# Kernel optimization log

Measured on AMD Instinct MI355X. Metric: run time of the kernel, lower is better.

The kernel has to match this reference:

```python
import jax, jax.numpy as jnp
import numpy as np

H = 64
B = 128
R_PER_G = 1024
P_PER_G = 2048
R = B * R_PER_G      # 131072 routers
P = B * P_PER_G      # 262144 packets
E_PASS = 1048576     # packet -> router
E_TRANS = 1048576    # router -> packet
E_CONN = 524288      # router -> router
NUM_LABELS = 11      # label_max - label_min


def setup_inputs() -> dict:
    key = jax.random.key(0)
    ks = jax.random.split(key, 40)
    f32 = jnp.float32

    def w(k, shape):
        fan_in = shape[0]
        return (jax.random.normal(k, shape, f32) / np.sqrt(fan_in)).astype(f32)

    inp = {}
    # graph node features
    inp['freq'] = jax.random.uniform(ks[0], (P, 1), f32)
    inp['flit'] = jax.random.normal(ks[1], (P, 32), f32)
    inp['op_type'] = jax.random.uniform(ks[2], (R, 4), f32)
    # edge lists (src, dst) per etype
    inp['pass_src'] = jax.random.randint(ks[3], (E_PASS,), 0, P, jnp.int32)
    inp['pass_dst'] = jax.random.randint(ks[4], (E_PASS,), 0, R, jnp.int32)
    inp['transfer_src'] = jax.random.randint(ks[5], (E_TRANS,), 0, R, jnp.int32)
    inp['transfer_dst'] = jax.random.randint(ks[6], (E_TRANS,), 0, P, jnp.int32)
    inp['connect_src'] = jax.random.randint(ks[7], (E_CONN,), 0, R, jnp.int32)
    inp['connect_dst'] = jax.random.randint(ks[8], (E_CONN,), 0, R, jnp.int32)
    # graph id of each router node (batched graphs, contiguous)
    inp['router_gid'] = jnp.repeat(jnp.arange(B, dtype=jnp.int32), R_PER_G)
    # FeatureGen params
    inp['Wf'] = w(ks[10], (1, H));      inp['bf'] = jnp.zeros((H,), f32)
    inp['Wl'] = w(ks[11], (32, H));     inp['bl'] = jnp.zeros((H,), f32)
    inp['Wo'] = w(ks[12], (4, H));      inp['bo'] = jnp.zeros((H,), f32)
    inp['Wfh'] = w(ks[13], (2 * H, H)); inp['bfh'] = jnp.zeros((H,), f32)
    inp['Wfn'] = w(ks[14], (H, H));     inp['bfn'] = jnp.zeros((H,), f32)
    # conv1 / conv2 params
    inp['c1_Wr'] = w(ks[15], (2 * H, H)); inp['c1_br'] = jnp.zeros((H,), f32)
    inp['c1_Wp'] = w(ks[16], (H, H));     inp['c1_bp'] = jnp.zeros((H,), f32)
    inp['c2_Wr'] = w(ks[17], (2 * H, H)); inp['c2_br'] = jnp.zeros((H,), f32)
    inp['c2_Wp'] = w(ks[18], (H, H));     inp['c2_bp'] = jnp.zeros((H,), f32)
    # prediction head
    inp['h1W'] = w(ks[19], (2 * H, H));        inp['h1b'] = jnp.zeros((H,), f32)
    inp['h2W'] = w(ks[20], (H, H));            inp['h2b'] = jnp.zeros((H,), f32)
    inp['h3W'] = w(ks[21], (H, NUM_LABELS));   inp['h3b'] = jnp.zeros((NUM_LABELS,), f32)
    return inp


def _conv(r_feat, p_feat, pass_src, pass_dst, transfer_src, transfer_dst,
          connect_src, connect_dst, Wr, br, Wp, bp):
    relu = jax.nn.relu
    # 'pass': copy_u packet feat, sum at router -> h1
    h1 = jax.ops.segment_sum(p_feat[pass_src], pass_dst, num_segments=R)
    # 'connect': copy_u router feat, sum at router -> h2
    h2 = jax.ops.segment_sum(r_feat[connect_src], connect_dst, num_segments=R)
    # 'transfer': copy_u router feat, mean at packet -> h1
    msum = jax.ops.segment_sum(r_feat[transfer_src], transfer_dst, num_segments=P)
    cnt = jax.ops.segment_sum(jnp.ones((transfer_dst.shape[0],), r_feat.dtype),
                              transfer_dst, num_segments=P)
    pmean = msum / jnp.maximum(cnt, 1.0)[:, None]
    r_out = r_feat + relu(jnp.concatenate([h1, h2], axis=-1) @ Wr + br)
    p_out = p_feat + relu(pmean @ Wp + bp)
    return r_out, p_out


def reference(freq, flit, op_type, pass_src, pass_dst, transfer_src, transfer_dst,
              connect_src, connect_dst, router_gid,
              Wf, bf, Wl, bl, Wo, bo, Wfh, bfh, Wfn, bfn,
              c1_Wr, c1_br, c1_Wp, c1_bp, c2_Wr, c2_br, c2_Wp, c2_bp,
              h1W, h1b, h2W, h2b, h3W, h3b):
    relu = jax.nn.relu
    # FeatureGen
    freq_feat = relu(freq @ Wf + bf)                 # [P, H]
    flit_feat = relu(flit @ Wl + bl)                 # [P, H]
    p_feat = relu(jnp.concatenate([freq_feat, flit_feat], axis=1) @ Wfh + bfh)
    r_feat = relu(relu(op_type @ Wo + bo) @ Wfn + bfn)  # [R, H]
    # two hetero conv layers
    r_feat, p_feat = _conv(r_feat, p_feat, pass_src, pass_dst, transfer_src,
                           transfer_dst, connect_src, connect_dst,
                           c1_Wr, c1_br, c1_Wp, c1_bp)
    r_feat, p_feat = _conv(r_feat, p_feat, pass_src, pass_dst, transfer_src,
                           transfer_dst, connect_src, connect_dst,
                           c2_Wr, c2_br, c2_Wp, c2_bp)
    # per-graph readout over router nodes: sum and max
    emb_sum = jax.ops.segment_sum(r_feat, router_gid, num_segments=B)   # [B, H]
    emb_max = jax.ops.segment_max(r_feat, router_gid, num_segments=B)   # [B, H]
    emb = jnp.concatenate([emb_sum, emb_max], axis=-1)                  # [B, 2H]
    # prediction head
    h = relu(emb @ h1W + h1b)
    h = relu(h @ h2W + h2b)
    pred = h @ h3W + h3b                                                # [B, 11]
    return pred
```

## Files before the change

### kernel.cpp

```cpp
#include <hip/hip_runtime.h>
#include <cstddef>

#define RELU(x) ((x) > 0.f ? (x) : 0.f)

constexpr int PN = 262144;
constexpr int RN = 131072;
constexpr int BN = 128;
constexpr int EPASS = 1048576;
constexpr int ETRANS = 1048576;
constexpr int ECONN = 524288;

__device__ __forceinline__ float bflo(unsigned u) { return __uint_as_float(u << 16); }
__device__ __forceinline__ float bfhi(unsigned u) { return __uint_as_float(u & 0xffff0000u); }
__device__ __forceinline__ unsigned bfpk(float x, float y) {
    unsigned ux = __float_as_uint(x), uy = __float_as_uint(y);
    ux += 0x7fffu + ((ux >> 16) & 1u);
    uy += 0x7fffu + ((uy >> 16) & 1u);
    return (ux >> 16) | (uy & 0xffff0000u);
}

struct Acc8 {
    float a0,a1,a2,a3,a4,a5,a6,a7;
    __device__ __forceinline__ void zero(){a0=a1=a2=a3=a4=a5=a6=a7=0.f;}
    __device__ __forceinline__ void add(uint4 v){
        a0+=bflo(v.x); a1+=bfhi(v.x); a2+=bflo(v.y); a3+=bfhi(v.y);
        a4+=bflo(v.z); a5+=bfhi(v.z); a6+=bflo(v.w); a7+=bfhi(v.w);
    }
    __device__ __forceinline__ void scale(float s){a0*=s;a1*=s;a2*=s;a3*=s;a4*=s;a5*=s;a6*=s;a7*=s;}
    __device__ __forceinline__ uint4 pack() const {
        return make_uint4(bfpk(a0,a1), bfpk(a2,a3), bfpk(a4,a5), bfpk(a6,a7));
    }
};

__global__ __launch_bounds__(256) void k_hist3(
    const int* __restrict__ pass_dst, const int* __restrict__ cn_dst,
    const int* __restrict__ tr_dst, int* __restrict__ deg3)
{
    int e = blockIdx.x * 256 + threadIdx.x;
    if (e < EPASS)                  atomicAdd(&deg3[pass_dst[e]], 1);
    else if (e < EPASS + ECONN)     atomicAdd(&deg3[RN + cn_dst[e - EPASS]], 1);
    else                            atomicAdd(&deg3[2*RN + tr_dst[e - EPASS - ECONN]], 1);
}

__global__ __launch_bounds__(1024) void k_scan_a(
    const int* __restrict__ deg3, int* __restrict__ rp_pass,
    int* __restrict__ rp_conn, int* __restrict__ rp_trans, int* __restrict__ bsum)
{
    int gb = blockIdx.x, t = threadIdx.x;
    const int* d; int* rp; int off;
    if (gb < 128)      { d = deg3;        rp = rp_pass;  off = gb * 1024; }
    else if (gb < 256) { d = deg3 + RN;   rp = rp_conn;  off = (gb-128) * 1024; }
    else               { d = deg3 + 2*RN; rp = rp_trans; off = (gb-256) * 1024; }
    int v = d[off + t];
    __shared__ int ss[1024];
    ss[t] = v;
    __syncthreads();
    for (int dd = 1; dd < 1024; dd <<= 1) {
        int u = (t >= dd) ? ss[t-dd] : 0;
        __syncthreads();
        ss[t] += u;
        __syncthreads();
    }
    rp[off + t] = ss[t] - v;
    if (t == 1023) bsum[gb] = ss[t];
}

__global__ __launch_bounds__(256) void k_scan_b(int* __restrict__ bsum)
{
    int s = blockIdx.x, t = threadIdx.x;
    int base = (s == 0) ? 0 : (s == 1 ? 128 : 256);
    int n = (s == 2) ? 256 : 128;
    int v = (t < n) ? bsum[base + t] : 0;
    __shared__ int ss[256];
    ss[t] = v;
    __syncthreads();
    for (int dd = 1; dd < 256; dd <<= 1) {
        int u = (t >= dd) ? ss[t-dd] : 0;
        __syncthreads();
        ss[t] += u;
        __syncthreads();
    }
    if (t < n) bsum[base + t] = ss[t] - v;
}

__global__ __launch_bounds__(1024) void k_scan_c(
    int* __restrict__ rp_pass, int* __restrict__ rp_conn, int* __restrict__ rp_trans,
    const int* __restrict__ bsum)
{
    int gb = blockIdx.x, t = threadIdx.x;
    int* rp; int off;
    if (gb < 128)      { rp = rp_pass;  off = gb * 1024; }
    else if (gb < 256) { rp = rp_conn;  off = (gb-128) * 1024; }
    else               { rp = rp_trans; off = (gb-256) * 1024; }
    rp[off + t] += bsum[gb];
    if (t == 0) {
        if (gb == 0)   rp_pass[RN]  = EPASS;
        if (gb == 128) rp_conn[RN]  = ECONN;
        if (gb == 256) rp_trans[PN] = ETRANS;
    }
}

__global__ __launch_bounds__(256) void k_fill3(
    const int* __restrict__ pass_src, const int* __restrict__ pass_dst,
    const int* __restrict__ cn_src,   const int* __restrict__ cn_dst,
    const int* __restrict__ tr_src,   const int* __restrict__ tr_dst,
    const int* __restrict__ rp_pass, const int* __restrict__ rp_conn,
    const int* __restrict__ rp_trans, int* __restrict__ cur3,
    int* __restrict__ csrc_pass, int* __restrict__ csrc_conn, int* __restrict__ csrc_trans)
{
    int e = blockIdx.x * 256 + threadIdx.x;
    if (e < EPASS) {
        int d = pass_dst[e];
        int pos = atomicAdd(&cur3[d], 1);
        csrc_pass[rp_pass[d] + pos] = pass_src[e];
    } else if (e < EPASS + ECONN) {
        int ee = e - EPASS;
        int d = cn_dst[ee];
        int pos = atomicAdd(&cur3[RN + d], 1);
        csrc_conn[rp_conn[d] + pos] = cn_src[ee];
    } else {
        int ee = e - EPASS - ECONN;
        int d = tr_dst[ee];
        int pos = atomicAdd(&cur3[2*RN + d], 1);
        csrc_trans[rp_trans[d] + pos] = tr_src[ee];
    }
}

__global__ __launch_bounds__(256) void k_gather_r(
    const ushort* __restrict__ pf, const ushort* __restrict__ rfv,
    const int* __restrict__ rp_pass, const int* __restrict__ csrc_pass,
    const int* __restrict__ rp_conn, const int* __restrict__ csrc_conn,
    ushort* __restrict__ h12)
{
    int tid = blockIdx.x * 256 + threadIdx.x;
    int n = tid >> 3, c = tid & 7;
    Acc8 a;
    {
        int beg = rp_pass[n], end = rp_pass[n + 1];
        a.zero();
        int j = beg;
        for (; j + 4 <= end; j += 4) {
            int s0 = csrc_pass[j], s1 = csrc_pass[j+1], s2 = csrc_pass[j+2], s3 = csrc_pass[j+3];
            uint4 v0 = *(const uint4*)(pf + (size_t)s0 * 64 + c * 8);
            uint4 v1 = *(const uint4*)(pf + (size_t)s1 * 64 + c * 8);
            uint4 v2 = *(const uint4*)(pf + (size_t)s2 * 64 + c * 8);
            uint4 v3 = *(const uint4*)(pf + (size_t)s3 * 64 + c * 8);
            a.add(v0); a.add(v1); a.add(v2); a.add(v3);
        }
        for (; j < end; ++j) {
            int s0 = csrc_pass[j];
            a.add(*(const uint4*)(pf + (size_t)s0 * 64 + c * 8));
        }
        *(uint4*)(h12 + (size_t)n * 128 + c * 8) = a.pack();
    }
    {
        int beg = rp_conn[n], end = rp_conn[n + 1];
        a.zero();
        int j = beg;
        for (; j + 4 <= end; j += 4) {
            int s0 = csrc_conn[j], s1 = csrc_conn[j+1], s2 = csrc_conn[j+2], s3 = csrc_conn[j+3];
            uint4 v0 = *(const uint4*)(rfv + (size_t)s0 * 64 + c * 8);
            uint4 v1 = *(const uint4*)(rfv + (size_t)s1 * 64 + c * 8);
            uint4 v2 = *(const uint4*)(rfv + (size_t)s2 * 64 + c * 8);
            uint4 v3 = *(const uint4*)(rfv + (size_t)s3 * 64 + c * 8);
            a.add(v0); a.add(v1); a.add(v2); a.add(v3);
        }
        for (; j < end; ++j) {
            int s0 = csrc_conn[j];
            a.add(*(const uint4*)(rfv + (size_t)s0 * 64 + c * 8));
        }
        *(uint4*)(h12 + (size_t)n * 128 + 64 + c * 8) = a.pack();
    }
}

__global__ __launch_bounds__(256) void k_gather_t(
    const ushort* __restrict__ rfv, const int* __restrict__ rp_trans,
    const int* __restrict__ csrc_trans, ushort* __restrict__ pmean)
{
    int tid = blockIdx.x * 256 + threadIdx.x;
    int n = tid >> 3, c = tid & 7;
    int beg = rp_trans[n], end = rp_trans[n + 1];
    Acc8 a;
    a.zero();
    int j = beg;
    for (; j + 4 <= end; j += 4) {
        int s0 = csrc_trans[j], s1 = csrc_trans[j+1], s2 = csrc_trans[j+2], s3 = csrc_trans[j+3];
        uint4 v0 = *(const uint4*)(rfv + (size_t)s0 * 64 + c * 8);
        uint4 v1 = *(const uint4*)(rfv + (size_t)s1 * 64 + c * 8);
        uint4 v2 = *(const uint4*)(rfv + (size_t)s2 * 64 + c * 8);
        uint4 v3 = *(const uint4*)(rfv + (size_t)s3 * 64 + c * 8);
        a.add(v0); a.add(v1); a.add(v2); a.add(v3);
    }
    for (; j < end; ++j) {
        int s0 = csrc_trans[j];
        a.add(*(const uint4*)(rfv + (size_t)s0 * 64 + c * 8));
    }
    a.scale(1.0f / fmaxf((float)(end - beg), 1.0f));
    *(uint4*)(pmean + (size_t)n * 64 + c * 8) = a.pack();
}

__global__ __launch_bounds__(256) void k_pfeat(
    const float* __restrict__ freq, const float* __restrict__ flit,
    const float* __restrict__ Wf, const float* __restrict__ bf,
    const float* __restrict__ Wl, const float* __restrict__ bl,
    const float* __restrict__ Wfh, const float* __restrict__ bfh,
    ushort* __restrict__ pf)
{
    __shared__ float sWlT[64*32];
    __shared__ float sWfh[128*64];
    __shared__ float sWf[64], sbf[64], sbl[64], sbfh[64];
    for (int i = threadIdx.x; i < 64*32; i += 256) {
        int j = i >> 5, k = i & 31;
        sWlT[i] = Wl[k*64 + j];
    }
    for (int i = threadIdx.x; i < 128*64; i += 256) sWfh[i] = Wfh[i];
    if (threadIdx.x < 64) {
        sWf[threadIdx.x]  = Wf[threadIdx.x];
        sbf[threadIdx.x]  = bf[threadIdx.x];
        sbl[threadIdx.x]  = bl[threadIdx.x];
        sbfh[threadIdx.x] = bfh[threadIdx.x];
    }
    __syncthreads();
    int p = blockIdx.x * 256 + threadIdx.x;
    float fl[32];
    const float4* fsrc = (const float4*)(flit + (size_t)p * 32);
    #pragma unroll
    for (int q = 0; q < 8; ++q) {
        float4 v = fsrc[q];
        fl[q*4+0]=v.x; fl[q*4+1]=v.y; fl[q*4+2]=v.z; fl[q*4+3]=v.w;
    }
    float fr = freq[p];
    float out[64];
    #pragma unroll
    for (int h = 0; h < 64; ++h) out[h] = sbfh[h];
    for (int j = 0; j < 64; ++j) {
        const float* wrow = &sWlT[j*32];
        float a0 = sbl[j], a1 = 0.f, a2 = 0.f, a3 = 0.f;
        #pragma unroll
        for (int k = 0; k < 8; ++k) {
            a0 += fl[k]    * wrow[k];
            a1 += fl[k+8]  * wrow[k+8];
            a2 += fl[k+16] * wrow[k+16];
            a3 += fl[k+24] * wrow[k+24];
        }
        float cj = RELU((a0+a1)+(a2+a3));
        #pragma unroll
        for (int h = 0; h < 64; ++h) out[h] += cj * sWfh[(64+j)*64+h];
    }
    for (int j = 0; j < 64; ++j) {
        float cj = RELU(fr * sWf[j] + sbf[j]);
        #pragma unroll
        for (int h = 0; h < 64; ++h) out[h] += cj * sWfh[j*64+h];
    }
    uint4* op4 = (uint4*)(pf + (size_t)p * 64);
    #pragma unroll
    for (int q = 0; q < 8; ++q) {
        op4[q] = make_uint4(bfpk(RELU(out[8*q+0]), RELU(out[8*q+1])),
                            bfpk(RELU(out[8*q+2]), RELU(out[8*q+3])),
                            bfpk(RELU(out[8*q+4]), RELU(out[8*q+5])),
                            bfpk(RELU(out[8*q+6]), RELU(out[8*q+7])));
    }
}

__global__ __launch_bounds__(256) void k_rfeat(
    const float* __restrict__ op,
    const float* __restrict__ Wo, const float* __restrict__ bo,
    const float* __restrict__ Wfn, const float* __restrict__ bfn,
    ushort* __restrict__ rf)
{
    __shared__ float sWoT[64*4];
    __shared__ float sWfn[64*64], sbo[64], sbfn[64];
    for (int i = threadIdx.x; i < 64*4; i += 256) {
        int j = i >> 2, d = i & 3;
        sWoT[i] = Wo[d*64 + j];
    }
    for (int i = threadIdx.x; i < 64*64; i += 256) sWfn[i] = Wfn[i];
    if (threadIdx.x < 64) { sbo[threadIdx.x] = bo[threadIdx.x]; sbfn[threadIdx.x] = bfn[threadIdx.x]; }
    __syncthreads();
    int r = blockIdx.x * 256 + threadIdx.x;
    float4 o4 = *(const float4*)(op + (size_t)r * 4);
    float out[64];
    #pragma unroll
    for (int h = 0; h < 64; ++h) out[h] = sbfn[h];
    for (int j = 0; j < 64; ++j) {
        const float4 w = *(const float4*)&sWoT[j*4];
        float tj = RELU(o4.x*w.x + o4.y*w.y + o4.z*w.z + o4.w*w.w + sbo[j]);
        #pragma unroll
        for (int h = 0; h < 64; ++h) out[h] += tj * sWfn[j*64+h];
    }
    uint4* op4 = (uint4*)(rf + (size_t)r * 64);
    #pragma unroll
    for (int q = 0; q < 8; ++q) {
        op4[q] = make_uint4(bfpk(RELU(out[8*q+0]), RELU(out[8*q+1])),
                            bfpk(RELU(out[8*q+2]), RELU(out[8*q+3])),
                            bfpk(RELU(out[8*q+4]), RELU(out[8*q+5])),
                            bfpk(RELU(out[8*q+6]), RELU(out[8*q+7])));
    }
}

__global__ __launch_bounds__(256) void k_rupd(
    const ushort* __restrict__ h12,
    const float* __restrict__ Wr, const float* __restrict__ br,
    ushort* __restrict__ rf)
{
    __shared__ float sW[128*64], sb[64];
    for (int i = threadIdx.x; i < 128*64; i += 256) sW[i] = Wr[i];
    if (threadIdx.x < 64) sb[threadIdx.x] = br[threadIdx.x];
    __syncthreads();
    int r = blockIdx.x * 256 + threadIdx.x;
    const uint4* hp = (const uint4*)(h12 + (size_t)r * 128);
    float out[64];
    #pragma unroll
    for (int h = 0; h < 64; ++h) out[h] = sb[h];
    for (int q = 0; q < 16; ++q) {
        uint4 v = hp[q];
        float x0 = bflo(v.x), x1 = bfhi(v.x), x2 = bflo(v.y), x3 = bfhi(v.y);
        float x4 = bflo(v.z), x5 = bfhi(v.z), x6 = bflo(v.w), x7 = bfhi(v.w);
        const float* w = &sW[(8*q)*64];
        #pragma unroll
        for (int h = 0; h < 64; ++h) {
            out[h] += x0*w[h] + x1*w[64+h] + x2*w[128+h] + x3*w[192+h]
                    + x4*w[256+h] + x5*w[320+h] + x6*w[384+h] + x7*w[448+h];
        }
    }
    uint4* rp4 = (uint4*)(rf + (size_t)r * 64);
    #pragma unroll
    for (int q = 0; q < 8; ++q) {
        uint4 cur = rp4[q];
        float c0 = bflo(cur.x) + RELU(out[8*q+0]), c1 = bfhi(cur.x) + RELU(out[8*q+1]);
        float c2 = bflo(cur.y) + RELU(out[8*q+2]), c3 = bfhi(cur.y) + RELU(out[8*q+3]);
        float c4 = bflo(cur.z) + RELU(out[8*q+4]), c5 = bfhi(cur.z) + RELU(out[8*q+5]);
        float c6 = bflo(cur.w) + RELU(out[8*q+6]), c7 = bfhi(cur.w) + RELU(out[8*q+7]);
        rp4[q] = make_uint4(bfpk(c0,c1), bfpk(c2,c3), bfpk(c4,c5), bfpk(c6,c7));
    }
}

__global__ __launch_bounds__(256) void k_pupd(
    const ushort* __restrict__ pmean,
    const float* __restrict__ Wp, const float* __restrict__ bp,
    ushort* __restrict__ pf)
{
    __shared__ float sW[64*64], sb[64];
    for (int i = threadIdx.x; i < 64*64; i += 256) sW[i] = Wp[i];
    if (threadIdx.x < 64) sb[threadIdx.x] = bp[threadIdx.x];
    __syncthreads();
    int p = blockIdx.x * 256 + threadIdx.x;
    const uint4* mp = (const uint4*)(pmean + (size_t)p * 64);
    float out[64];
    #pragma unroll
    for (int h = 0; h < 64; ++h) out[h] = sb[h];
    for (int q = 0; q < 8; ++q) {
        uint4 v = mp[q];
        float x0 = bflo(v.x), x1 = bfhi(v.x), x2 = bflo(v.y), x3 = bfhi(v.y);
        float x4 = bflo(v.z), x5 = bfhi(v.z), x6 = bflo(v.w), x7 = bfhi(v.w);
        const float* w = &sW[(8*q)*64];
        #pragma unroll
        for (int h = 0; h < 64; ++h) {
            out[h] += x0*w[h] + x1*w[64+h] + x2*w[128+h] + x3*w[192+h]
                    + x4*w[256+h] + x5*w[320+h] + x6*w[384+h] + x7*w[448+h];
        }
    }
    uint4* pp4 = (uint4*)(pf + (size_t)p * 64);
    #pragma unroll
    for (int q = 0; q < 8; ++q) {
        uint4 cur = pp4[q];
        float c0 = bflo(cur.x) + RELU(out[8*q+0]), c1 = bfhi(cur.x) + RELU(out[8*q+1]);
        float c2 = bflo(cur.y) + RELU(out[8*q+2]), c3 = bfhi(cur.y) + RELU(out[8*q+3]);
        float c4 = bflo(cur.z) + RELU(out[8*q+4]), c5 = bfhi(cur.z) + RELU(out[8*q+5]);
        float c6 = bflo(cur.w) + RELU(out[8*q+6]), c7 = bfhi(cur.w) + RELU(out[8*q+7]);
        pp4[q] = make_uint4(bfpk(c0,c1), bfpk(c2,c3), bfpk(c4,c5), bfpk(c6,c7));
    }
}

__global__ __launch_bounds__(256) void k_head(
    const ushort* __restrict__ rf,
    const float* __restrict__ h1W, const float* __restrict__ h1b,
    const float* __restrict__ h2W, const float* __restrict__ h2b,
    const float* __restrict__ h3W, const float* __restrict__ h3b,
    float* __restrict__ out)
{
    int b = blockIdx.x;
    int tid = threadIdx.x;
    int h = tid & 63, part = tid >> 6;
    const ushort* base = rf + (size_t)b * 1024 * 64;
    float s = 0.f, m = -3.0e38f;
    #pragma unroll 8
    for (int r = part * 256; r < part * 256 + 256; ++r) {
        float v = bflo((unsigned)base[(size_t)r * 64 + h]);
        s += v;
        m = fmaxf(m, v);
    }
    __shared__ float ssum[4][64], smax[4][64];
    __shared__ float emb[128], hid1[64], hid2[64];
    ssum[part][h] = s;
    smax[part][h] = m;
    __syncthreads();
    if (tid < 64) {
        emb[tid] = ssum[0][tid] + ssum[1][tid] + ssum[2][tid] + ssum[3][tid];
    } else if (tid < 128) {
        int hh = tid - 64;
        emb[64+hh] = fmaxf(fmaxf(smax[0][hh], smax[1][hh]), fmaxf(smax[2][hh], smax[3][hh]));
    }
    __syncthreads();
    if (tid < 64) {
        float a = h1b[tid];
        #pragma unroll
        for (int j = 0; j < 128; ++j) a += emb[j] * h1W[j*64 + tid];
        hid1[tid] = RELU(a);
    }
    __syncthreads();
    if (tid < 64) {
        float a = h2b[tid];
        #pragma unroll
        for (int j = 0; j < 64; ++j) a += hid1[j] * h2W[j*64 + tid];
        hid2[tid] = RELU(a);
    }
    __syncthreads();
    if (tid < 11) {
        float a = h3b[tid];
        #pragma unroll
        for (int j = 0; j < 64; ++j) a += hid2[j] * h3W[j*11 + tid];
        out[(size_t)b * 11 + tid] = a;
    }
}

extern "C" void kernel_launch(void* const* d_in, const int* in_sizes, int n_in,
                              void* d_out, int out_size, void* d_ws, size_t ws_size,
                              hipStream_t stream)
{
    const float* freq = (const float*)d_in[0];
    const float* flit = (const float*)d_in[1];
    const float* op   = (const float*)d_in[2];
    const int* pass_src = (const int*)d_in[3];
    const int* pass_dst = (const int*)d_in[4];
    const int* tr_src   = (const int*)d_in[5];
    const int* tr_dst   = (const int*)d_in[6];
    const int* cn_src   = (const int*)d_in[7];
    const int* cn_dst   = (const int*)d_in[8];
    const float* Wf  = (const float*)d_in[10]; const float* bf  = (const float*)d_in[11];
    const float* Wl  = (const float*)d_in[12]; const float* bl  = (const float*)d_in[13];
    const float* Wo  = (const float*)d_in[14]; const float* bo  = (const float*)d_in[15];
    const float* Wfh = (const float*)d_in[16]; const float* bfh = (const float*)d_in[17];
    const float* Wfn = (const float*)d_in[18]; const float* bfn = (const float*)d_in[19];
    const float* c1_Wr = (const float*)d_in[20]; const float* c1_br = (const float*)d_in[21];
    const float* c1_Wp = (const float*)d_in[22]; const float* c1_bp = (const float*)d_in[23];
    const float* c2_Wr = (const float*)d_in[24]; const float* c2_br = (const float*)d_in[25];
    const float* c2_Wp = (const float*)d_in[26]; const float* c2_bp = (const float*)d_in[27];
    const float* h1W = (const float*)d_in[28]; const float* h1b = (const float*)d_in[29];
    const float* h2W = (const float*)d_in[30]; const float* h2b = (const float*)d_in[31];
    const float* h3W = (const float*)d_in[32]; const float* h3b = (const float*)d_in[33];

    ushort* pf    = (ushort*)d_ws;
    ushort* rfv   = pf    + (size_t)PN * 64;
    ushort* h12   = rfv   + (size_t)RN * 64;
    ushort* pmean = h12   + (size_t)RN * 128;
    int* rp_pass  = (int*)(pmean + (size_t)PN * 64);
    int* rp_conn  = rp_pass  + (RN + 64);
    int* rp_trans = rp_conn  + (RN + 64);
    int* deg3     = rp_trans + (PN + 64);
    int* cur3     = deg3 + (2*RN + PN);
    int* bsum     = cur3 + (2*RN + PN);
    int* csrc_pass  = bsum + 512 + 64;
    int* csrc_conn  = csrc_pass + EPASS;
    int* csrc_trans = csrc_conn + ECONN;

    hipMemsetAsync(deg3, 0, (size_t)(2*RN + PN) * 2 * 4, stream);
    k_hist3<<<(EPASS+ECONN+ETRANS)/256, 256, 0, stream>>>(pass_dst, cn_dst, tr_dst, deg3);
    k_scan_a<<<512, 1024, 0, stream>>>(deg3, rp_pass, rp_conn, rp_trans, bsum);
    k_scan_b<<<3, 256, 0, stream>>>(bsum);
    k_scan_c<<<512, 1024, 0, stream>>>(rp_pass, rp_conn, rp_trans, bsum);
    k_fill3<<<(EPASS+ECONN+ETRANS)/256, 256, 0, stream>>>(
        pass_src, pass_dst, cn_src, cn_dst, tr_src, tr_dst,
        rp_pass, rp_conn, rp_trans, cur3, csrc_pass, csrc_conn, csrc_trans);

    k_pfeat<<<PN/256, 256, 0, stream>>>(freq, flit, Wf, bf, Wl, bl, Wfh, bfh, pf);
    k_rfeat<<<RN/256, 256, 0, stream>>>(op, Wo, bo, Wfn, bfn, rfv);

    k_gather_r<<<RN*8/256, 256, 0, stream>>>(pf, rfv, rp_pass, csrc_pass, rp_conn, csrc_conn, h12);
    k_gather_t<<<PN*8/256, 256, 0, stream>>>(rfv, rp_trans, csrc_trans, pmean);
    k_rupd<<<RN/256, 256, 0, stream>>>(h12, c1_Wr, c1_br, rfv);
    k_pupd<<<PN/256, 256, 0, stream>>>(pmean, c1_Wp, c1_bp, pf);

    k_gather_r<<<RN*8/256, 256, 0, stream>>>(pf, rfv, rp_pass, csrc_pass, rp_conn, csrc_conn, h12);
    k_gather_t<<<PN*8/256, 256, 0, stream>>>(rfv, rp_trans, csrc_trans, pmean);
    k_rupd<<<RN/256, 256, 0, stream>>>(h12, c2_Wr, c2_br, rfv);
    k_pupd<<<PN/256, 256, 0, stream>>>(pmean, c2_Wp, c2_bp, pf);

    k_head<<<BN, 256, 0, stream>>>(rfv, h1W, h1b, h2W, h2b, h3W, h3b, (float*)d_out);
}
```

Baseline: 959.4 us.

## Use bf16 MFMA for router and packet update matmuls

Rewrites k_rupd and k_pupd to compute the dense linear layers with 16x16x32 bf16 MFMA instructions instead of per-thread scalar FMA loops over shared fp32 weights. Weights are converted to bf16 and transposed into padded shared memory, and each wave handles 16 rows, so grids grow to N/64 blocks. This removes the heavy scalar ALU and register cost of 64-wide accumulators. In exchange, weights are rounded to bf16, and the residual read-modify-write becomes scattered 2-byte accesses instead of 16-byte vector accesses.

```diff
diff --git a/kernel.cpp b/kernel.cpp
--- a/kernel.cpp
+++ b/kernel.cpp
@@ -9,6 +9,9 @@
 constexpr int EPASS = 1048576;
 constexpr int ETRANS = 1048576;
 constexpr int ECONN = 524288;
+
+typedef short bf16x8 __attribute__((ext_vector_type(8)));
+typedef float f32x4  __attribute__((ext_vector_type(4)));
 
 __device__ __forceinline__ float bflo(unsigned u) { return __uint_as_float(u << 16); }
 __device__ __forceinline__ float bfhi(unsigned u) { return __uint_as_float(u & 0xffff0000u); }
@@ -17,6 +20,11 @@
     ux += 0x7fffu + ((ux >> 16) & 1u);
     uy += 0x7fffu + ((uy >> 16) & 1u);
     return (ux >> 16) | (uy & 0xffff0000u);
+}
+__device__ __forceinline__ unsigned bfpk1(float x) {
+    unsigned u = __float_as_uint(x);
+    u += 0x7fffu + ((u >> 16) & 1u);
+    return u >> 16;
 }
 
 struct Acc8 {
@@ -299,76 +307,104 @@
 }
 
 __global__ __launch_bounds__(256) void k_rupd(
-    const ushort* __restrict__ h12,
-    const float* __restrict__ Wr, const float* __restrict__ br,
-    ushort* __restrict__ rf)
-{
-    __shared__ float sW[128*64], sb[64];
-    for (int i = threadIdx.x; i < 128*64; i += 256) sW[i] = Wr[i];
+    const ushort* __restrict__ h12, const float* __restrict__ Wr,
+    const float* __restrict__ br, ushort* __restrict__ rf)
+{
+    __shared__ ushort sW[64*136];
+    __shared__ float sb[64];
+    uint* sWu = (uint*)sW;
+    for (int u = threadIdx.x; u < 64*64; u += 256) {
+        int n = u >> 6, kp = u & 63;
+        unsigned lo = bfpk1(Wr[(2*kp)*64 + n]);
+        unsigned hi = bfpk1(Wr[(2*kp+1)*64 + n]);
+        sWu[n*68 + kp] = lo | (hi << 16);
+    }
     if (threadIdx.x < 64) sb[threadIdx.x] = br[threadIdx.x];
     __syncthreads();
-    int r = blockIdx.x * 256 + threadIdx.x;
-    const uint4* hp = (const uint4*)(h12 + (size_t)r * 128);
-    float out[64];
-    #pragma unroll
-    for (int h = 0; h < 64; ++h) out[h] = sb[h];
-    for (int q = 0; q < 16; ++q) {
-        uint4 v = hp[q];
-        float x0 = bflo(v.x), x1 = bfhi(v.x), x2 = bflo(v.y), x3 = bfhi(v.y);
-        float x4 = bflo(v.z), x5 = bfhi(v.z), x6 = bflo(v.w), x7 = bfhi(v.w);
-        const float* w = &sW[(8*q)*64];
-        #pragma unroll
-        for (int h = 0; h < 64; ++h) {
-            out[h] += x0*w[h] + x1*w[64+h] + x2*w[128+h] + x3*w[192+h]
-                    + x4*w[256+h] + x5*w[320+h] + x6*w[384+h] + x7*w[448+h];
-        }
-    }
-    uint4* rp4 = (uint4*)(rf + (size_t)r * 64);
-    #pragma unroll
-    for (int q = 0; q < 8; ++q) {
-        uint4 cur = rp4[q];
-        float c0 = bflo(cur.x) + RELU(out[8*q+0]), c1 = bfhi(cur.x) + RELU(out[8*q+1]);
-        float c2 = bflo(cur.y) + RELU(out[8*q+2]), c3 = bfhi(cur.y) + RELU(out[8*q+3]);
-        float c4 = bflo(cur.z) + RELU(out[8*q+4]), c5 = bfhi(cur.z) + RELU(out[8*q+5]);
-        float c6 = bflo(cur.w) + RELU(out[8*q+6]), c7 = bfhi(cur.w) + RELU(out[8*q+7]);
-        rp4[q] = make_uint4(bfpk(c0,c1), bfpk(c2,c3), bfpk(c4,c5), bfpk(c6,c7));
+    int w = threadIdx.x >> 6, l = threadIdx.x & 63;
+    int nb = blockIdx.x * 64 + w * 16;
+    int m = l & 15, grp = l >> 4;
+    bf16x8 B[4][4];
+    #pragma unroll
+    for (int s = 0; s < 4; ++s)
+        #pragma unroll
+        for (int nt = 0; nt < 4; ++nt) {
+            int n = nt*16 + m;
+            B[s][nt] = *(const bf16x8*)&sW[n*136 + s*32 + grp*8];
+        }
+    f32x4 acc0 = {0,0,0,0}, acc1 = {0,0,0,0}, acc2 = {0,0,0,0}, acc3 = {0,0,0,0};
+    const ushort* xrow = h12 + (size_t)(nb + m) * 128;
+    #pragma unroll
+    for (int s = 0; s < 4; ++s) {
+        bf16x8 A = *(const bf16x8*)&xrow[s*32 + grp*8];
+        acc0 = __builtin_amdgcn_mfma_f32_16x16x32_bf16(A, B[s][0], acc0, 0, 0, 0);
+        acc1 = __builtin_amdgcn_mfma_f32_16x16x32_bf16(A, B[s][1], acc1, 0, 0, 0);
+        acc2 = __builtin_amdgcn_mfma_f32_16x16x32_bf16(A, B[s][2], acc2, 0, 0, 0);
+        acc3 = __builtin_amdgcn_mfma_f32_16x16x32_bf16(A, B[s][3], acc3, 0, 0, 0);
+    }
+    #pragma unroll
+    for (int nt = 0; nt < 4; ++nt) {
+        int col = nt*16 + m;
+        float bias = sb[col];
+        #pragma unroll
+        for (int r = 0; r < 4; ++r) {
+            float v = (nt == 0) ? acc0[r] : (nt == 1) ? acc1[r] : (nt == 2) ? acc2[r] : acc3[r];
+            float u = RELU(v + bias);
+            ushort* ptr = rf + (size_t)(nb + grp*4 + r) * 64 + col;
+            float cur = bflo((unsigned)*ptr);
+            *ptr = (ushort)bfpk1(cur + u);
+        }
     }
 }
 
 __global__ __launch_bounds__(256) void k_pupd(
-    const ushort* __restrict__ pmean,
-    const float* __restrict__ Wp, const float* __restrict__ bp,
-    ushort* __restrict__ pf)
-{
-    __shared__ float sW[64*64], sb[64];
-    for (int i = threadIdx.x; i < 64*64; i += 256) sW[i] = Wp[i];
+    const ushort* __restrict__ pmean, const float* __restrict__ Wp,
+    const float* __restrict__ bp, ushort* __restrict__ pf)
+{
+    __shared__ ushort sW[64*72];
+    __shared__ float sb[64];
+    uint* sWu = (uint*)sW;
+    for (int u = threadIdx.x; u < 64*32; u += 256) {
+        int n = u >> 5, kp = u & 31;
+        unsigned lo = bfpk1(Wp[(2*kp)*64 + n]);
+        unsigned hi = bfpk1(Wp[(2*kp+1)*64 + n]);
+        sWu[n*36 + kp] = lo | (hi << 16);
+    }
     if (threadIdx.x < 64) sb[threadIdx.x] = bp[threadIdx.x];
     __syncthreads();
-    int p = blockIdx.x * 256 + threadIdx.x;
-    const uint4* mp = (const uint4*)(pmean + (size_t)p * 64);
-    float out[64];
-    #pragma unroll
-    for (int h = 0; h < 64; ++h) out[h] = sb[h];
-    for (int q = 0; q < 8; ++q) {
-        uint4 v = mp[q];
-        float x0 = bflo(v.x), x1 = bfhi(v.x), x2 = bflo(v.y), x3 = bfhi(v.y);
-        float x4 = bflo(v.z), x5 = bfhi(v.z), x6 = bflo(v.w), x7 = bfhi(v.w);
-        const float* w = &sW[(8*q)*64];
-        #pragma unroll
-        for (int h = 0; h < 64; ++h) {
-            out[h] += x0*w[h] + x1*w[64+h] + x2*w[128+h] + x3*w[192+h]
-                    + x4*w[256+h] + x5*w[320+h] + x6*w[384+h] + x7*w[448+h];
-        }
-    }
-    uint4* pp4 = (uint4*)(pf + (size_t)p * 64);
-    #pragma unroll
-    for (int q = 0; q < 8; ++q) {
-        uint4 cur = pp4[q];
-        float c0 = bflo(cur.x) + RELU(out[8*q+0]), c1 = bfhi(cur.x) + RELU(out[8*q+1]);
-        float c2 = bflo(cur.y) + RELU(out[8*q+2]), c3 = bfhi(cur.y) + RELU(out[8*q+3]);
-        float c4 = bflo(cur.z) + RELU(out[8*q+4]), c5 = bfhi(cur.z) + RELU(out[8*q+5]);
-        float c6 = bflo(cur.w) + RELU(out[8*q+6]), c7 = bfhi(cur.w) + RELU(out[8*q+7]);
-        pp4[q] = make_uint4(bfpk(c0,c1), bfpk(c2,c3), bfpk(c4,c5), bfpk(c6,c7));
+    int w = threadIdx.x >> 6, l = threadIdx.x & 63;
+    int nb = blockIdx.x * 64 + w * 16;
+    int m = l & 15, grp = l >> 4;
+    bf16x8 B[2][4];
+    #pragma unroll
+    for (int s = 0; s < 2; ++s)
+        #pragma unroll
+        for (int nt = 0; nt < 4; ++nt) {
+            int n = nt*16 + m;
+            B[s][nt] = *(const bf16x8*)&sW[n*72 + s*32 + grp*8];
+        }
+    f32x4 acc0 = {0,0,0,0}, acc1 = {0,0,0,0}, acc2 = {0,0,0,0}, acc3 = {0,0,0,0};
+    const ushort* xrow = pmean + (size_t)(nb + m) * 64;
+    #pragma unroll
+    for (int s = 0; s < 2; ++s) {
+        bf16x8 A = *(const bf16x8*)&xrow[s*32 + grp*8];
+        acc0 = __builtin_amdgcn_mfma_f32_16x16x32_bf16(A, B[s][0], acc0, 0, 0, 0);
+        acc1 = __builtin_amdgcn_mfma_f32_16x16x32_bf16(A, B[s][1], acc1, 0, 0, 0);
+        acc2 = __builtin_amdgcn_mfma_f32_16x16x32_bf16(A, B[s][2], acc2, 0, 0, 0);
+        acc3 = __builtin_amdgcn_mfma_f32_16x16x32_bf16(A, B[s][3], acc3, 0, 0, 0);
+    }
+    #pragma unroll
+    for (int nt = 0; nt < 4; ++nt) {
+        int col = nt*16 + m;
+        float bias = sb[col];
+        #pragma unroll
+        for (int r = 0; r < 4; ++r) {
+            float v = (nt == 0) ? acc0[r] : (nt == 1) ? acc1[r] : (nt == 2) ? acc2[r] : acc3[r];
+            float u = RELU(v + bias);
+            ushort* ptr = pf + (size_t)(nb + grp*4 + r) * 64 + col;
+            float cur = bflo((unsigned)*ptr);
+            *ptr = (ushort)bfpk1(cur + u);
+        }
     }
 }
 
@@ -478,13 +514,13 @@
 
     k_gather_r<<<RN*8/256, 256, 0, stream>>>(pf, rfv, rp_pass, csrc_pass, rp_conn, csrc_conn, h12);
     k_gather_t<<<PN*8/256, 256, 0, stream>>>(rfv, rp_trans, csrc_trans, pmean);
-    k_rupd<<<RN/256, 256, 0, stream>>>(h12, c1_Wr, c1_br, rfv);
-    k_pupd<<<PN/256, 256, 0, stream>>>(pmean, c1_Wp, c1_bp, pf);
+    k_rupd<<<RN/64, 256, 0, stream>>>(h12, c1_Wr, c1_br, rfv);
+    k_pupd<<<PN/64, 256, 0, stream>>>(pmean, c1_Wp, c1_bp, pf);
 
     k_gather_r<<<RN*8/256, 256, 0, stream>>>(pf, rfv, rp_pass, csrc_pass, rp_conn, csrc_conn, h12);
     k_gather_t<<<PN*8/256, 256, 0, stream>>>(rfv, rp_trans, csrc_trans, pmean);
-    k_rupd<<<RN/256, 256, 0, stream>>>(h12, c2_Wr, c2_br, rfv);
-    k_pupd<<<PN/256, 256, 0, stream>>>(pmean, c2_Wp, c2_bp, pf);
+    k_rupd<<<RN/64, 256, 0, stream>>>(h12, c2_Wr, c2_br, rfv);
+    k_pupd<<<PN/64, 256, 0, stream>>>(pmean, c2_Wp, c2_bp, pf);
 
     k_head<<<BN, 256, 0, stream>>>(rfv, h1W, h1b, h2W, h2b, h3W, h3b, (float*)d_out);
 }
```

Measured after the change: 883.6 us. 1.09x faster.
